# Kernel optimization log

Measured on AMD Instinct MI355X. Metric: run time of the kernel, lower is better.

The kernel has to match this reference:

```python
import jax, jax.numpy as jnp
import numpy as np

T = 4
THRESH = 1.0
TAU = 1.0
GAMA = 0.5

# Heaviside spike with Gaussian surrogate gradient (SgNormal)
@jax.custom_vjp
def sg_normal(x):
    return (x > 0).astype(x.dtype)

def _sg_fwd(x):
    return (x > 0).astype(x.dtype), x

def _sg_bwd(x, g):
    inv_norm = 1.0 / (GAMA * np.sqrt(2.0 * np.pi).astype(np.float32))
    return (g * jnp.exp(-(x * x) / (2.0 * GAMA * GAMA)) * inv_norm,)

sg_normal.defvjp(_sg_fwd, _sg_bwd)


def setup_inputs() -> dict:
    key = jax.random.key(0)
    x = jax.random.normal(key, (T, 64, 128, 32, 32), dtype=jnp.float32)
    return {"x": x}


def reference(x):
    # LIF recurrence over T timesteps: mem = mem*tau + x[t]; spike = H(mem - thresh); mem = (1-spike)*mem
    def step(mem, xt):
        mem = mem * TAU + xt
        spike = sg_normal(mem - THRESH)
        mem = (1.0 - spike) * mem
        return mem, spike

    mem0 = jnp.zeros(x.shape[1:], dtype=x.dtype)
    _, spikes = jax.lax.scan(step, mem0, x)  # spikes: [T, B, C, H, W]
    return spikes
```

## Files before the change

kernel.cpp:

```cpp
#include <hip/hip_runtime.h>


#define LIF_T 4

typedef float v4f __attribute__((ext_vector_type(4)));

__global__ __launch_bounds__(256) void
lif_spike_kernel(const float* __restrict__ x, float* __restrict__ out, int n_vec, int n) {
    int v = blockIdx.x * blockDim.x + threadIdx.x;
    if (v >= n_vec) return;
    size_t i = (size_t)v * 4;

    v4f xt[LIF_T];
#pragma unroll
    for (int t = 0; t < LIF_T; ++t) {
        xt[t] = *reinterpret_cast<const v4f*>(x + (size_t)t * n + i);
    }

    v4f sp[LIF_T];
    v4f mem = (v4f)(0.0f);
#pragma unroll
    for (int t = 0; t < LIF_T; ++t) {
        mem += xt[t];
        v4f s;
        s.x = (mem.x > 1.0f) ? 1.0f : 0.0f;
        s.y = (mem.y > 1.0f) ? 1.0f : 0.0f;
        s.z = (mem.z > 1.0f) ? 1.0f : 0.0f;
        s.w = (mem.w > 1.0f) ? 1.0f : 0.0f;
        sp[t] = s;
        mem.x = (s.x > 0.f) ? 0.f : mem.x;
        mem.y = (s.y > 0.f) ? 0.f : mem.y;
        mem.z = (s.z > 0.f) ? 0.f : mem.z;
        mem.w = (s.w > 0.f) ? 0.f : mem.w;
    }

#pragma unroll
    for (int t = 0; t < LIF_T; ++t) {
        __builtin_nontemporal_store(sp[t], reinterpret_cast<v4f*>(out + (size_t)t * n + i));
    }
}

extern "C" void kernel_launch(void* const* d_in, const int* in_sizes, int n_in,
                              void* d_out, int out_size, void* d_ws, size_t ws_size,
                              hipStream_t stream) {
    const float* x = (const float*)d_in[0];
    float* out = (float*)d_out;

    int n = out_size / LIF_T;
    int n_vec = n / 4;

    int block = 256;
    int grid = (n_vec + block - 1) / block;
    lif_spike_kernel<<<grid, block, 0, stream>>>(x, out, n_vec, n);
}
```

Before: 236.7 us.

## Use persistent grid-stride loop with software-prefetched loads for LIF kernel

Replaces the one-thread-per-vector launch with a fixed grid of 2048 blocks that stride over the data. Each iteration loads the next four timestep vectors before computing and storing the current ones, so loads overlap with stores. Stores are now issued inside the timestep loop rather than buffered. The kernel is purely bandwidth bound, so prefetching and fewer blocks may not help, and the grid-stride loop can reduce memory-level parallelism.

```diff
diff --git a/kernel.cpp b/kernel.cpp
--- a/kernel.cpp
+++ b/kernel.cpp
@@ -5,19 +5,9 @@
 
 typedef float v4f __attribute__((ext_vector_type(4)));
 
-__global__ __launch_bounds__(256) void
-lif_spike_kernel(const float* __restrict__ x, float* __restrict__ out, int n_vec, int n) {
-    int v = blockIdx.x * blockDim.x + threadIdx.x;
-    if (v >= n_vec) return;
-    size_t i = (size_t)v * 4;
-
-    v4f xt[LIF_T];
-#pragma unroll
-    for (int t = 0; t < LIF_T; ++t) {
-        xt[t] = *reinterpret_cast<const v4f*>(x + (size_t)t * n + i);
-    }
-
-    v4f sp[LIF_T];
+__device__ __forceinline__ void lif_compute_store(const v4f xt[LIF_T],
+                                                  float* __restrict__ out,
+                                                  int n, size_t col) {
     v4f mem = (v4f)(0.0f);
 #pragma unroll
     for (int t = 0; t < LIF_T; ++t) {
@@ -27,17 +17,43 @@
         s.y = (mem.y > 1.0f) ? 1.0f : 0.0f;
         s.z = (mem.z > 1.0f) ? 1.0f : 0.0f;
         s.w = (mem.w > 1.0f) ? 1.0f : 0.0f;
-        sp[t] = s;
         mem.x = (s.x > 0.f) ? 0.f : mem.x;
         mem.y = (s.y > 0.f) ? 0.f : mem.y;
         mem.z = (s.z > 0.f) ? 0.f : mem.z;
         mem.w = (s.w > 0.f) ? 0.f : mem.w;
+        __builtin_nontemporal_store(s, reinterpret_cast<v4f*>(out + (size_t)t * n + col));
+    }
+}
+
+__global__ __launch_bounds__(256, 8) void
+lif_spike_kernel(const float* __restrict__ x, float* __restrict__ out, int n_vec, int n) {
+    const int tid     = blockIdx.x * blockDim.x + threadIdx.x;
+    const int nthread = gridDim.x * blockDim.x;
+
+    int idx = tid;
+    if (idx >= n_vec) return;
+
+    v4f cur[LIF_T];
+#pragma unroll
+    for (int t = 0; t < LIF_T; ++t) {
+        cur[t] = *reinterpret_cast<const v4f*>(x + (size_t)t * n + (size_t)idx * 4);
     }
 
+    for (int nidx = idx + nthread; nidx < n_vec; nidx += nthread) {
+        v4f nxt[LIF_T];
 #pragma unroll
-    for (int t = 0; t < LIF_T; ++t) {
-        __builtin_nontemporal_store(sp[t], reinterpret_cast<v4f*>(out + (size_t)t * n + i));
+        for (int t = 0; t < LIF_T; ++t) {
+            nxt[t] = *reinterpret_cast<const v4f*>(x + (size_t)t * n + (size_t)nidx * 4);
+        }
+
+        lif_compute_store(cur, out, n, (size_t)idx * 4);
+
+#pragma unroll
+        for (int t = 0; t < LIF_T; ++t) cur[t] = nxt[t];
+        idx = nidx;
     }
+
+    lif_compute_store(cur, out, n, (size_t)idx * 4);
 }
 
 extern "C" void kernel_launch(void* const* d_in, const int* in_sizes, int n_in,
@@ -50,6 +66,6 @@
     int n_vec = n / 4;
 
     int block = 256;
-    int grid = (n_vec + block - 1) / block;
+    int grid  = 2048;
     lif_spike_kernel<<<grid, block, 0, stream>>>(x, out, n_vec, n);
 }
```

New measurement: 239.9 us. Within noise of the previous version (+1.3%).
